# Kernel optimization log

Measured on AMD Instinct MI355X. Metric: run time of the kernel, lower is better.

The kernel has to match this reference:

```python
import jax, jax.numpy as jnp
import numpy as np

HEAD_SIZE = 64


def q_shift_multihead(x, ph, pw, head_dim=HEAD_SIZE, shift=1):
    # x: [B, T, C], T == ph*pw. Quarter-wise spatial shifts per head channel block.
    B, T, C = x.shape
    a = jnp.transpose(x, (0, 2, 1)).reshape(B, C // head_dim, head_dim, ph, pw)
    q = head_dim // 4
    out = jnp.zeros_like(a)
    out = out.at[:, :, 0:q, :, shift:].set(a[:, :, 0:q, :, :-shift])          # shift right in W
    out = out.at[:, :, q:2 * q, :, :-shift].set(a[:, :, q:2 * q, :, shift:])  # shift left in W
    out = out.at[:, :, 2 * q:3 * q, shift:, :].set(a[:, :, 2 * q:3 * q, :-shift, :])  # shift down in H
    out = out.at[:, :, 3 * q:, :-shift, :].set(a[:, :, 3 * q:, shift:, :])            # shift up in H
    return jnp.transpose(out.reshape(B, C, T), (0, 2, 1))


def wkv6(r, k, v, w, u):
    # RWKV-6 linear recurrence. r,k,v,w: [B,T,C]; u: [H, hs]. Decay applied as exp(-exp(w)).
    B, T, C = r.shape
    H, hs = C // HEAD_SIZE, HEAD_SIZE
    rh = jnp.transpose(r.reshape(B, T, H, hs), (1, 0, 2, 3))
    kh = jnp.transpose(k.reshape(B, T, H, hs), (1, 0, 2, 3))
    vh = jnp.transpose(v.reshape(B, T, H, hs), (1, 0, 2, 3))
    wh = jnp.exp(-jnp.exp(jnp.transpose(w.reshape(B, T, H, hs), (1, 0, 2, 3))))

    def step(S, inp):  # S: [B,H,hs(key j),hs(val i)]
        rt, kt, vt, wt = inp
        kv = kt[..., :, None] * vt[..., None, :]                # [B,H,hs,hs]
        y = jnp.einsum('bhj,bhji->bhi', rt, S + u[None, :, :, None] * kv)
        return wt[..., None] * S + kv, y

    S0 = jnp.zeros((B, H, hs, hs), r.dtype)
    _, ys = jax.lax.scan(step, S0, (rh, kh, vh, wh))
    return jnp.transpose(ys, (1, 0, 2, 3)).reshape(B, T, C)


def group_norm(x, weight, bias, n_groups, eps=1e-5):
    # x: [N, C]
    N, C = x.shape
    g = x.reshape(N, n_groups, C // n_groups)
    mu = g.mean(-1, keepdims=True)
    var = ((g - mu) ** 2).mean(-1, keepdims=True)
    g = (g - mu) / jnp.sqrt(var + eps)
    return g.reshape(N, C) * weight + bias


def setup_inputs() -> dict:
    key = jax.random.key(0)
    B, ph, pw, C = 8, 32, 32, 768
    T = ph * pw
    n_layer, layer_id = 12, 6
    H = C // HEAD_SIZE
    ks = jax.random.split(key, 10)
    x = jax.random.normal(ks[0], (B, T, C), jnp.float32)
    W_r = 0.02 * jax.random.normal(ks[1], (C, C), jnp.float32)
    W_k = 0.02 * jax.random.normal(ks[2], (C, C), jnp.float32)
    W_v = 0.02 * jax.random.normal(ks[3], (C, C), jnp.float32)
    W_g = 0.02 * jax.random.normal(ks[4], (C, C), jnp.float32)
    W_o = 0.02 * jax.random.normal(ks[5], (C, C), jnp.float32)
    r01 = layer_id / (n_layer - 1)
    r10 = 1.0 - layer_id / n_layer
    ddd = np.arange(C, dtype=np.float64) / C
    maa_x = jnp.asarray(1.0 - ddd ** r10, jnp.float32).reshape(1, 1, C)
    maa_w = maa_x
    maa_k = maa_x
    maa_v = jnp.asarray(1.0 - (ddd ** r10 + 0.3 * r01), jnp.float32).reshape(1, 1, C)
    maa_r = jnp.asarray(1.0 - ddd ** (0.5 * r10), jnp.float32).reshape(1, 1, C)
    maa_g = maa_r
    maa_w1 = jax.random.uniform(ks[6], (C, 32 * 5), jnp.float32, -1e-4, 1e-4)
    maa_w2 = jax.random.uniform(ks[7], (5, 32, C), jnp.float32, -1e-4, 1e-4)
    n = np.arange(C, dtype=np.float64)
    time_decay = jnp.asarray(-6 + 5 * (n / (C - 1)) ** (0.7 + 1.3 * r01), jnp.float32).reshape(1, 1, C)
    dec_w1 = jax.random.uniform(ks[8], (C, 64), jnp.float32, -1e-4, 1e-4)
    dec_w2 = jax.random.uniform(ks[9], (64, C), jnp.float32, -1e-4, 1e-4)
    zig = ((n + 1) % 3 - 1) * 0.1
    faaaa = jnp.asarray(r01 * (1 - n / (C - 1)) + zig, jnp.float32).reshape(H, HEAD_SIZE)
    ln_w = jnp.ones((C,), jnp.float32)
    ln_b = jnp.zeros((C,), jnp.float32)
    return dict(x=x, W_r=W_r, W_k=W_k, W_v=W_v, W_g=W_g, W_o=W_o,
                maa_x=maa_x, maa_w=maa_w, maa_k=maa_k, maa_v=maa_v, maa_r=maa_r, maa_g=maa_g,
                maa_w1=maa_w1, maa_w2=maa_w2, time_decay=time_decay,
                dec_w1=dec_w1, dec_w2=dec_w2, faaaa=faaaa, ln_w=ln_w, ln_b=ln_b,
                patch_h=ph, patch_w=pw)


def reference(x, W_r, W_k, W_v, W_g, W_o, maa_x, maa_w, maa_k, maa_v, maa_r, maa_g,
              maa_w1, maa_w2, time_decay, dec_w1, dec_w2, faaaa, ln_w, ln_b,
              patch_h, patch_w):
    B, T, C = x.shape
    xx = q_shift_multihead(x, patch_h, patch_w) - x
    xxx = x + xx * maa_x
    t = jnp.tanh(xxx @ maa_w1).reshape(B, T, 5, 32)
    m = jnp.einsum('btfr,frc->fbtc', t, maa_w2)  # [5,B,T,C]
    mw, mk, mv, mr, mg = m[0], m[1], m[2], m[3], m[4]
    xw = x + xx * (maa_w + mw)
    xk = x + xx * (maa_k + mk)
    xv = x + xx * (maa_v + mv)
    xr = x + xx * (maa_r + mr)
    xg = x + xx * (maa_g + mg)
    r = xr @ W_r.T
    k = xk @ W_k.T
    v = xv @ W_v.T
    g = jax.nn.relu(xg @ W_g.T)
    ww = jnp.tanh(xw @ dec_w1) @ dec_w2
    w = time_decay + ww
    y = wkv6(r, k, v, w, faaaa)
    y = group_norm(y.reshape(B * T, C), ln_w, ln_b, C // HEAD_SIZE).reshape(B, T, C)
    return (y * g) @ W_o.T
```

## Files before the change

kernel.cpp:

```cpp
#include <hip/hip_runtime.h>
#include <math.h>


#define EPI_NONE 0
#define EPI_TANH 1
#define EPI_RELU 2
#define EPI_BIAS 3

typedef float f32x4 __attribute__((ext_vector_type(4)));
typedef __bf16 bf16x8 __attribute__((ext_vector_type(8)));

__device__ __forceinline__ ushort f2bf(float x) {
  unsigned u = __float_as_uint(x);
  return (ushort)((u + 0x7fffu + ((u >> 16) & 1u)) >> 16);
}

#define GLDS16(gp, lp)                                                   \
  __builtin_amdgcn_global_load_lds(                                      \
      (const __attribute__((address_space(1))) void*)(gp),               \
      (__attribute__((address_space(3))) void*)(lp), 16, 0, 0)

__global__ __launch_bounds__(256) void k_qshift(
    const float* __restrict__ x, const float* __restrict__ maa_x,
    ushort* __restrict__ xxx_bf,
    int B, int T, int C, int ph, int pw) {
  long idx = (long)blockIdx.x * blockDim.x + threadIdx.x;
  long total = (long)B * T * C;
  if (idx >= total) return;
  int c = (int)(idx % C);
  long bt = idx / C;
  int t = (int)(bt % T);
  int quarter = (c & 63) >> 4;
  int hh = t / pw;
  int ww = t - hh * pw;
  long rowbase = (bt - t) * C;
  float sval = 0.f;
  int st = -1;
  if (quarter == 0)      { if (ww >= 1)      st = t - 1;  }
  else if (quarter == 1) { if (ww < pw - 1)  st = t + 1;  }
  else if (quarter == 2) { if (hh >= 1)      st = t - pw; }
  else                   { if (hh < ph - 1)  st = t + pw; }
  if (st >= 0) sval = x[rowbase + (long)st * C + c];
  float xval = x[idx];
  float d = sval - xval;
  xxx_bf[idx] = f2bf(xval + d * maa_x[c]);
}

__global__ __launch_bounds__(256) void k_wprep(
    const float* __restrict__ w1, const float* __restrict__ w2,
    const float* __restrict__ dw1, const float* __restrict__ dw2,
    ushort* __restrict__ maa1T, ushort* __restrict__ w2T,
    ushort* __restrict__ w1dT, ushort* __restrict__ w2dT) {
  int idx = blockIdx.x * 256 + threadIdx.x;
  if (idx < 196608) {
    int n = idx / 768, k = idx - n * 768;
    maa1T[idx] = f2bf(n < 160 ? w1[(size_t)k * 160 + n] : 0.f);
  } else if (idx < 196608 + 122880) {
    int j = idx - 196608;
    int c = j / 160, kk = j - c * 160;
    w2T[j] = f2bf(w2[(size_t)kk * 768 + c]);
  } else if (idx < 196608 + 122880 + 98304) {
    int j = idx - (196608 + 122880);
    int n = j / 768, k = j - n * 768;
    w1dT[j] = f2bf(n < 64 ? dw1[(size_t)k * 64 + n] : 0.f);
  } else {
    int j = idx - (196608 + 122880 + 98304);
    int n = j >> 6, k = j & 63;
    w2dT[j] = f2bf(dw2[(size_t)k * 768 + n]);
  }
}

__global__ __launch_bounds__(256) void k_mix5m(
    const ushort* __restrict__ t5b, const ushort* __restrict__ w2T,
    const float* __restrict__ x,
    const float* __restrict__ maa_w, const float* __restrict__ maa_k,
    const float* __restrict__ maa_v, const float* __restrict__ maa_r,
    const float* __restrict__ maa_g,
    ushort* __restrict__ xw, ushort* __restrict__ xk, ushort* __restrict__ xvb,
    ushort* __restrict__ xr, ushort* __restrict__ xg,
    int C, int T, int ph, int pw) {
  int tid = threadIdx.x;
  int lane = tid & 63, wid = tid >> 6;
  int m0 = blockIdx.y * 64, n0 = blockIdx.x * 128;
  int lm = lane & 15, lk = (lane >> 4) * 8;
  int rq = (lane >> 4) * 4;
  const ushort* ap = t5b + (size_t)(m0 + wid * 16 + lm) * 160 + lk;

  int stq[4][4];
#pragma unroll
  for (int q = 0; q < 4; q++) {
    int mr = m0 + wid * 16 + rq + q;
    int t = mr % T;
    int hh = t / pw, ww = t - hh * pw;
    stq[q][0] = (ww >= 1)      ? mr - 1  : -1;
    stq[q][1] = (ww < pw - 1)  ? mr + 1  : -1;
    stq[q][2] = (hh >= 1)      ? mr - pw : -1;
    stq[q][3] = (hh < ph - 1)  ? mr + pw : -1;
  }

  float xh[8][4], dh[8][4];
#pragma unroll
  for (int j = 0; j < 8; j++)
#pragma unroll
    for (int q = 0; q < 4; q++) {
      int mr = m0 + wid * 16 + rq + q;
      int col = n0 + j * 16 + lm;
      float xv = x[(size_t)mr * C + col];
      int sr = stq[q][j & 3];
      float sv = (sr >= 0) ? x[(size_t)sr * C + col] : 0.f;
      xh[j][q] = xv;
      dh[j][q] = sv - xv;
    }

#pragma unroll
  for (int f = 0; f < 5; f++) {
    bf16x8 af = *(const bf16x8*)(ap + f * 32);
    f32x4 acc[8];
#pragma unroll
    for (int j = 0; j < 8; j++) {
      bf16x8 bfj = *(const bf16x8*)(w2T +
          (size_t)(n0 + j * 16 + lm) * 160 + f * 32 + lk);
      acc[j] = __builtin_amdgcn_mfma_f32_16x16x32_bf16(
          af, bfj, (f32x4){0.f, 0.f, 0.f, 0.f}, 0, 0, 0);
    }
    const float* maa_f = (f == 0) ? maa_w : (f == 1) ? maa_k
                        : (f == 2) ? maa_v : (f == 3) ? maa_r : maa_g;
    ushort* dst = (f == 0) ? xw : (f == 1) ? xk
                 : (f == 2) ? xvb : (f == 3) ? xr : xg;
#pragma unroll
    for (int j = 0; j < 8; j++) {
      float mf = maa_f[n0 + j * 16 + lm];
#pragma unroll
      for (int q = 0; q < 4; q++) {
        size_t off = (size_t)(m0 + wid * 16 + rq + q) * C + (n0 + j * 16 + lm);
        dst[off] = f2bf(xh[j][q] + dh[j][q] * (mf + acc[j][q]));
      }
    }
  }
}

__global__ __launch_bounds__(256) void k_cvt5(
    const float* __restrict__ s0, const float* __restrict__ s1,
    const float* __restrict__ s2, const float* __restrict__ s3,
    const float* __restrict__ s4,
    ushort* __restrict__ d0, ushort* __restrict__ d1,
    ushort* __restrict__ d2, ushort* __restrict__ d3,
    ushort* __restrict__ d4, int n) {
  const float* s;
  ushort* d;
  switch (blockIdx.y) {
    case 0: s = s0; d = d0; break;
    case 1: s = s1; d = d1; break;
    case 2: s = s2; d = d2; break;
    case 3: s = s3; d = d3; break;
    default: s = s4; d = d4; break;
  }
  int i = (blockIdx.x * 256 + threadIdx.x) * 4;
  if (i >= n) return;
  float4 v = *(const float4*)(s + i);
  ushort4 o;
  o.x = f2bf(v.x); o.y = f2bf(v.y); o.z = f2bf(v.z); o.w = f2bf(v.w);
  *(ushort4*)(d + i) = o;
}

template <int EPI, bool NMASK, bool OBF16>
__global__ __launch_bounds__(256) void k_gemm_bf(
    const ushort* __restrict__ A, const ushort* __restrict__ W,
    const float* __restrict__ bias, void* __restrict__ Cm,
    int M, int N, int K) {
  __shared__ ushort Al[128 * 64];
  __shared__ ushort Bl[128 * 64];
  int nwg = gridDim.x * gridDim.y;
  int bid = blockIdx.y * gridDim.x + blockIdx.x;
  int swz = (nwg & 7) == 0 ? ((bid & 7) * (nwg >> 3) + (bid >> 3)) : bid;
  int bx = swz % gridDim.x, by = swz / gridDim.x;
  int m0 = by * 128, n0 = bx * 128;
  int tid = threadIdx.x;
  int lane = tid & 63, wave = tid >> 6;
  int wm = (wave >> 1) * 64, wn = (wave & 1) * 64;
  int lm = lane & 15, g = lane >> 4;
  f32x4 acc[4][4];
#pragma unroll
  for (int i = 0; i < 4; i++)
#pragma unroll
    for (int j = 0; j < 4; j++) acc[i][j] = (f32x4){0.f, 0.f, 0.f, 0.f};

  for (int k0 = 0; k0 < K; k0 += 64) {
#pragma unroll
    for (int i = 0; i < 4; i++) {
      int cid = tid + i * 256;
      int row = cid >> 3, p = cid & 7;
      int cq = p ^ (row & 7);
      GLDS16(A + (size_t)(m0 + row) * K + k0 + cq * 8, Al + cid * 8);
      GLDS16(W + (size_t)(n0 + row) * K + k0 + cq * 8, Bl + cid * 8);
    }
    __syncthreads();
#pragma unroll
    for (int s = 0; s < 2; s++) {
      bf16x8 af[4], bf[4];
#pragma unroll
      for (int i = 0; i < 4; i++) {
        int r = wm + i * 16 + lm;
        af[i] = *(const bf16x8*)&Al[r * 64 + (((s * 4 + g) ^ (r & 7)) * 8)];
        int rb = wn + i * 16 + lm;
        bf[i] = *(const bf16x8*)&Bl[rb * 64 + (((s * 4 + g) ^ (rb & 7)) * 8)];
      }
#pragma unroll
      for (int i = 0; i < 4; i++)
#pragma unroll
        for (int j = 0; j < 4; j++)
          acc[i][j] = __builtin_amdgcn_mfma_f32_16x16x32_bf16(
              af[i], bf[j], acc[i][j], 0, 0, 0);
    }
    __syncthreads();
  }
  int rq = (lane >> 4) * 4;
#pragma unroll
  for (int i = 0; i < 4; i++) {
#pragma unroll
    for (int j = 0; j < 4; j++) {
      int gn = n0 + wn + j * 16 + lm;
      if (NMASK && gn >= N) continue;
      float bv = (EPI == EPI_BIAS) ? bias[gn] : 0.f;
#pragma unroll
      for (int q = 0; q < 4; q++) {
        int gm = m0 + wm + i * 16 + rq + q;
        float val = acc[i][j][q];
        if (EPI == EPI_BIAS) val += bv;
        if (EPI == EPI_RELU) val = fmaxf(val, 0.f);
        if (EPI == EPI_TANH) val = tanhf(val);
        if (OBF16) ((ushort*)Cm)[(size_t)gm * N + gn] = f2bf(val);
        else       ((float*)Cm)[(size_t)gm * N + gn] = val;
      }
    }
  }
}

__global__ __launch_bounds__(256) void k_proj4(
    const ushort* __restrict__ A0, const ushort* __restrict__ A1,
    const ushort* __restrict__ A2, const ushort* __restrict__ A3,
    const ushort* __restrict__ W0, const ushort* __restrict__ W1,
    const ushort* __restrict__ W2, const ushort* __restrict__ W3,
    float* __restrict__ C0, float* __restrict__ C1,
    float* __restrict__ C2, float* __restrict__ C3,
    int M, int N, int K) {
  int nwg = gridDim.x;
  int bid = blockIdx.x;
  int swz = (bid & 7) * (nwg >> 3) + (bid >> 3);
  int nxt = N / 128;
  int per_z = (M / 128) * nxt;
  int z = swz / per_z;
  int rem = swz - z * per_z;
  int my = rem / nxt, nx = rem - my * nxt;
  const ushort* A = (z == 0) ? A0 : (z == 1) ? A1 : (z == 2) ? A2 : A3;
  const ushort* W = (z == 0) ? W0 : (z == 1) ? W1 : (z == 2) ? W2 : W3;
  float* Cm       = (z == 0) ? C0 : (z == 1) ? C1 : (z == 2) ? C2 : C3;
  __shared__ ushort Al[128 * 64];
  __shared__ ushort Bl[128 * 64];
  int tid = threadIdx.x;
  int m0 = my * 128, n0 = nx * 128;
  int lane = tid & 63, wave = tid >> 6;
  int wm = (wave >> 1) * 64, wn = (wave & 1) * 64;
  int lm = lane & 15, g = lane >> 4;
  f32x4 acc[4][4];
#pragma unroll
  for (int i = 0; i < 4; i++)
#pragma unroll
    for (int j = 0; j < 4; j++) acc[i][j] = (f32x4){0.f, 0.f, 0.f, 0.f};

  for (int k0 = 0; k0 < K; k0 += 64) {
#pragma unroll
    for (int i = 0; i < 4; i++) {
      int cid = tid + i * 256;
      int row = cid >> 3, p = cid & 7;
      int cq = p ^ (row & 7);
      GLDS16(A + (size_t)(m0 + row) * K + k0 + cq * 8, Al + cid * 8);
      GLDS16(W + (size_t)(n0 + row) * K + k0 + cq * 8, Bl + cid * 8);
    }
    __syncthreads();
#pragma unroll
    for (int s = 0; s < 2; s++) {
      bf16x8 af[4], bf[4];
#pragma unroll
      for (int i = 0; i < 4; i++) {
        int r = wm + i * 16 + lm;
        af[i] = *(const bf16x8*)&Al[r * 64 + (((s * 4 + g) ^ (r & 7)) * 8)];
        int rb = wn + i * 16 + lm;
        bf[i] = *(const bf16x8*)&Bl[rb * 64 + (((s * 4 + g) ^ (rb & 7)) * 8)];
      }
#pragma unroll
      for (int i = 0; i < 4; i++)
#pragma unroll
        for (int j = 0; j < 4; j++)
          acc[i][j] = __builtin_amdgcn_mfma_f32_16x16x32_bf16(
              af[i], bf[j], acc[i][j], 0, 0, 0);
    }
    __syncthreads();
  }
  bool relu = (z == 3);
  int rq = (lane >> 4) * 4;
#pragma unroll
  for (int i = 0; i < 4; i++) {
#pragma unroll
    for (int j = 0; j < 4; j++) {
      int gn = n0 + wn + j * 16 + lm;
#pragma unroll
      for (int q = 0; q < 4; q++) {
        int gm = m0 + wm + i * 16 + rq + q;
        float val = acc[i][j][q];
        if (relu) val = fmaxf(val, 0.f);
        Cm[(size_t)gm * N + gn] = val;
      }
    }
  }
}

__global__ __launch_bounds__(64) void k_wkv_pre(
    const float* __restrict__ r, const float* __restrict__ k,
    const float* __restrict__ w, const float* __restrict__ u,
    float* __restrict__ rt, float* __restrict__ kt,
    float* __restrict__ aL, float* __restrict__ pdiag,
    int B, int T, int C, int H, int L) {
  __shared__ float pls[64 * 65];
  int nch = T / L;
  int blk = blockIdx.x;
  int bh = blk / nch, c = blk - bh * nch;
  int b = bh / H, h = bh - b * H;
  int j = threadIdx.x;
  float uj = u[h * 64 + j];
  float cum = 0.f;
  long base = ((long)b * T + (long)c * L) * C + h * 64 + j;
  for (int tau = 0; tau < L; tau++) {
    long off = base + (long)tau * C;
    float wv = w[off];
    float rv = r[off];
    float kv = k[off];
    float e = expf(wv);
    rt[off] = rv * expf(-cum);
    cum += e;
    kt[off] = kv * expf(cum);
    pls[tau * 65 + j] = rv * uj * kv;
  }
  aL[((long)bh * nch + c) * 64 + j] = expf(-cum);
  __syncthreads();
  float s0 = 0.f, s1 = 0.f, s2 = 0.f, s3 = 0.f;
#pragma unroll
  for (int q = 0; q < 16; q++) {
    float4 p4 = *(const float4*)(pls + j * 65 + q * 4);
    s0 += p4.x; s1 += p4.y; s2 += p4.z; s3 += p4.w;
  }
  pdiag[(long)bh * T + c * L + j] = (s0 + s1) + (s2 + s3);
}

__global__ __launch_bounds__(256) void k_wkv_kv(
    const float* __restrict__ kt, const float* __restrict__ v,
    float* __restrict__ kvb, int B, int T, int C, int H, int L) {
  int nch = T / L;
  int blk = blockIdx.x;
  int bh = blk / nch, c = blk - bh * nch;
  int b = bh / H, h = bh - b * H;
  __shared__ float Ks[64 * 64];
  __shared__ float Vs[64 * 64];
  int tid = threadIdx.x;
  int lane = tid & 63, jg = tid >> 6;
  long cbase = ((long)b * T + (long)c * L) * C + h * 64;
#pragma unroll
  for (int i = 0; i < 4; i++) {
    int chunk = jg * 4 + i;
    int row = chunk * 4 + (lane >> 4);
    int cq = lane & 15;
    GLDS16(kt + cbase + (long)row * C + cq * 4, Ks + chunk * 256);
    GLDS16(v + cbase + (long)row * C + cq * 4, Vs + chunk * 256);
  }
  __syncthreads();
  float acc[16];
#pragma unroll
  for (int q = 0; q < 16; q++) acc[q] = 0.f;
  for (int s = 0; s < 64; s++) {
    float vi = Vs[s * 64 + lane];
#pragma unroll
    for (int q4 = 0; q4 < 4; q4++) {
      float4 kk = *(const float4*)(Ks + s * 64 + jg * 16 + q4 * 4);
      acc[q4 * 4 + 0] = fmaf(kk.x, vi, acc[q4 * 4 + 0]);
      acc[q4 * 4 + 1] = fmaf(kk.y, vi, acc[q4 * 4 + 1]);
      acc[q4 * 4 + 2] = fmaf(kk.z, vi, acc[q4 * 4 + 2]);
      acc[q4 * 4 + 3] = fmaf(kk.w, vi, acc[q4 * 4 + 3]);
    }
  }
  float* out = kvb + ((long)bh * nch + c) * 4096;
#pragma unroll
  for (int q = 0; q < 16; q++) out[(jg * 16 + q) * 64 + lane] = acc[q];
}

__global__ __launch_bounds__(256) void k_wkv_scan(
    const float* __restrict__ kvb, const float* __restrict__ aL,
    float* __restrict__ Scb, int nch) {
  int bh = blockIdx.x >> 4;
  int e = ((blockIdx.x & 15) << 8) + threadIdx.x;
  float S = 0.f;
  for (int c = 0; c < nch; c++) {
    long cb = ((long)bh * nch + c) * 4096 + e;
    Scb[cb] = S;
    S = aL[((long)bh * nch + c) * 64 + (e >> 6)] * (S + kvb[cb]);
  }
}

__global__ __launch_bounds__(256, 5) void k_wkv_intra(
    const float* __restrict__ rt, const float* __restrict__ kt,
    const float* __restrict__ v, const float* __restrict__ pdiag,
    const float* __restrict__ Scb, const float* __restrict__ g,
    const float* __restrict__ ln_w, const float* __restrict__ ln_b,
    ushort* __restrict__ z, int B, int T, int C, int H, int L) {
  int nch = T / L;
  int blk = blockIdx.x;
  int bh = blk / nch, c = blk - bh * nch;
  int b = bh / H, h = bh - b * H;
  __shared__ float TA[64 * 64];
  __shared__ float TB[64 * 64];
  int tid = threadIdx.x;
  int lane = tid & 63, wid = tid >> 6;
  int tau = lane;
  long cbase = ((long)b * T + (long)c * L) * C + h * 64;
  const float* scp = Scb + ((long)bh * nch + c) * 4096;

#pragma unroll
  for (int i = 0; i < 4; i++) {
    int chunk = wid * 4 + i;
    int row = chunk * 4 + (lane >> 4);
    int cq = lane & 15;
    GLDS16(rt + cbase + (long)row * C + ((cq ^ (row & 15)) * 4),
           TA + chunk * 256);
    GLDS16(kt + cbase + (long)row * C + cq * 4, TB + chunk * 256);
  }
  __syncthreads();

  float4 rreg[16];
#pragma unroll
  for (int q = 0; q < 16; q++)
    rreg[q] = *(const float4*)(TA + tau * 64 + ((q ^ (tau & 15)) * 4));
  float pd = pdiag[(long)bh * T + c * L + tau];
  __syncthreads();

#pragma unroll
  for (int i = 0; i < 4; i++) {
    int chunk = wid * 4 + i;
    int row = chunk * 4 + (lane >> 4);
    GLDS16(v + cbase + (long)row * C + (lane & 15) * 4, TA + chunk * 256);
  }

  __builtin_amdgcn_s_setprio(1);
#pragma unroll 2
  for (int ss = 0; ss < 16; ss++) {
    int s = wid * 16 + ss;
    float a0 = 0.f, a1 = 0.f, a2 = 0.f, a3 = 0.f;
#pragma unroll
    for (int q = 0; q < 16; q++) {
      float4 kk = *(const float4*)(TB + s * 64 + q * 4);
      a0 = fmaf(rreg[q].x, kk.x, a0);
      a1 = fmaf(rreg[q].y, kk.y, a1);
      a2 = fmaf(rreg[q].z, kk.z, a2);
      a3 = fmaf(rreg[q].w, kk.w, a3);
    }
    float a = (a0 + a1) + (a2 + a3);
    float val = (s < tau) ? a : (s == tau ? pd : 0.f);
    TB[s * 64 + tau] = val;
  }
  __builtin_amdgcn_s_setprio(0);
  __syncthreads();

  int row0 = wid * 16 + ((lane >> 4) << 2);
  int c0 = (lane & 15) * 4;
  float4 acc0 = {0.f, 0.f, 0.f, 0.f};
  float4 acc1 = {0.f, 0.f, 0.f, 0.f};
  float4 acc2 = {0.f, 0.f, 0.f, 0.f};
  float4 acc3 = {0.f, 0.f, 0.f, 0.f};
#define FMA1(A, P, V4)                 \
  A.x = fmaf(P, V4.x, A.x);            \
  A.y = fmaf(P, V4.y, A.y);            \
  A.z = fmaf(P, V4.z, A.z);            \
  A.w = fmaf(P, V4.w, A.w);
  __builtin_amdgcn_s_setprio(1);
#pragma unroll 4
  for (int j = 0; j < 64; j++) {
    float4 pp = *(const float4*)(TB + j * 64 + row0);
    float4 vv = *(const float4*)(TA + j * 64 + c0);
    FMA1(acc0, pp.x, vv);
    FMA1(acc1, pp.y, vv);
    FMA1(acc2, pp.z, vv);
    FMA1(acc3, pp.w, vv);
  }
  __builtin_amdgcn_s_setprio(0);
  __syncthreads();

#define WRQ(SG)                                                          \
  {                                                                      \
    _Pragma("unroll") for (int qq = 0; qq < 16; qq++) {                  \
      const float* rp = (const float*)&rreg[(SG) * 4 + (qq >> 2)];       \
      TA[((SG) * 16 + qq) * 64 + tau] = rp[qq & 3];                      \
    }                                                                    \
  }
  if (wid == 0)      WRQ(0)
  else if (wid == 1) WRQ(1)
  else if (wid == 2) WRQ(2)
  else               WRQ(3)
#undef WRQ
  __syncthreads();

  __builtin_amdgcn_s_setprio(1);
#pragma unroll 4
  for (int j = 0; j < 64; j++) {
    float4 rr = *(const float4*)(TA + j * 64 + row0);
    float4 ssv = *(const float4*)(scp + j * 64 + c0);
    FMA1(acc0, rr.x, ssv);
    FMA1(acc1, rr.y, ssv);
    FMA1(acc2, rr.z, ssv);
    FMA1(acc3, rr.w, ssv);
  }
  __builtin_amdgcn_s_setprio(0);
#undef FMA1

  float4 lw4 = *(const float4*)(ln_w + h * 64 + c0);
  float4 lb4 = *(const float4*)(ln_b + h * 64 + c0);
#define GNROW(A, m)                                                        \
  {                                                                        \
    float s1 = (A.x + A.y) + (A.z + A.w);                                  \
    s1 += __shfl_xor(s1, 1, 64);                                           \
    s1 += __shfl_xor(s1, 2, 64);                                           \
    s1 += __shfl_xor(s1, 4, 64);                                           \
    s1 += __shfl_xor(s1, 8, 64);                                           \
    float mu = s1 * (1.f / 64.f);                                          \
    float4 dd;                                                             \
    dd.x = A.x - mu; dd.y = A.y - mu; dd.z = A.z - mu; dd.w = A.w - mu;    \
    float s2 = (dd.x * dd.x + dd.y * dd.y) + (dd.z * dd.z + dd.w * dd.w);  \
    s2 += __shfl_xor(s2, 1, 64);                                           \
    s2 += __shfl_xor(s2, 2, 64);                                           \
    s2 += __shfl_xor(s2, 4, 64);                                           \
    s2 += __shfl_xor(s2, 8, 64);                                           \
    float rstd = rsqrtf(s2 * (1.f / 64.f) + 1e-5f);                        \
    long off = cbase + (long)(row0 + m) * C + c0;                          \
    float4 g4 = *(const float4*)(g + off);                                 \
    ushort4 ob;                                                            \
    ob.x = f2bf((dd.x * rstd * lw4.x + lb4.x) * g4.x);                     \
    ob.y = f2bf((dd.y * rstd * lw4.y + lb4.y) * g4.y);                     \
    ob.z = f2bf((dd.z * rstd * lw4.z + lb4.z) * g4.z);                     \
    ob.w = f2bf((dd.w * rstd * lw4.w + lb4.w) * g4.w);                     \
    *(ushort4*)(z + off) = ob;                                             \
  }
  GNROW(acc0, 0)
  GNROW(acc1, 1)
  GNROW(acc2, 2)
  GNROW(acc3, 3)
#undef GNROW
}

extern "C" void kernel_launch(void* const* d_in, const int* in_sizes, int n_in,
                              void* d_out, int out_size, void* d_ws, size_t ws_size,
                              hipStream_t stream) {
  const int B = 8, T = 1024, C = 768, H = 12, ph = 32, pw = 32;
  const int M = B * T;
  const int L = 64, NCH = T / L;

  const float* x        = (const float*)d_in[0];
  const float* W_r      = (const float*)d_in[1];
  const float* W_k      = (const float*)d_in[2];
  const float* W_v      = (const float*)d_in[3];
  const float* W_g      = (const float*)d_in[4];
  const float* W_o      = (const float*)d_in[5];
  const float* maa_x    = (const float*)d_in[6];
  const float* maa_w    = (const float*)d_in[7];
  const float* maa_k    = (const float*)d_in[8];
  const float* maa_v    = (const float*)d_in[9];
  const float* maa_r    = (const float*)d_in[10];
  const float* maa_g    = (const float*)d_in[11];
  const float* maa_w1   = (const float*)d_in[12];
  const float* maa_w2   = (const float*)d_in[13];
  const float* time_dec = (const float*)d_in[14];
  const float* dec_w1   = (const float*)d_in[15];
  const float* dec_w2   = (const float*)d_in[16];
  const float* faaaa    = (const float*)d_in[17];
  const float* ln_w     = (const float*)d_in[18];
  const float* ln_b     = (const float*)d_in[19];

  float* ws = (float*)d_ws;
  const size_t S = (size_t)M * C;
  float* F0 = ws + 0 * S;
  float* F1 = ws + 1 * S;
  float* F2 = ws + 2 * S;
  float* F3 = ws + 3 * S;
  float* F4 = ws + 4 * S;
  float* F5 = ws + 5 * S;
  float* F6 = ws + 6 * S;
  float* t5    = ws + 7 * S;
  float* t6    = t5 + (size_t)M * 160;
  float* aLb   = t6 + (size_t)M * 64;
  float* pdiag = aLb + (size_t)B * H * NCH * 64;
  float* dec_t = pdiag + (size_t)B * H * T;

  ushort* xxx_bf = (ushort*)F1;
  ushort* xw_bf = (ushort*)F2;
  ushort* xr_bf = (ushort*)F5;
  ushort* xk_bf = xr_bf + S;
  ushort* xv_bf = (ushort*)F6;
  ushort* xg_bf = xv_bf + S;
  ushort* z_bf  = (ushort*)F6;
  ushort* t5b   = (ushort*)t5;
  ushort* t_bf  = (ushort*)dec_t;
  ushort* w2T   = t_bf + (size_t)M * 64;
  float* kvb = F0;
  float* Scb = F1;
  const int WSZ = C * C;
  ushort* wr_bf = (ushort*)t5;
  ushort* wk_bf = wr_bf + WSZ;
  ushort* wv_bf = wk_bf + WSZ;
  ushort* wg_bf = wv_bf + WSZ;
  ushort* wo_bf = (ushort*)t6;
  ushort* maa1T = wo_bf + WSZ;
  ushort* w1dT  = maa1T + 256 * 768;
  ushort* w2dT  = w1dT + 128 * 768;

  {
    long total = (long)M * C;
    k_qshift<<<(int)((total + 255) / 256), 256, 0, stream>>>(
        x, maa_x, xxx_bf, B, T, C, ph, pw);
  }
  {
    k_wprep<<<1824, 256, 0, stream>>>(maa_w1, maa_w2, dec_w1, dec_w2,
                                      maa1T, w2T, w1dT, w2dT);
    dim3 grid(2, M / 128);
    k_gemm_bf<EPI_TANH, true, true><<<grid, 256, 0, stream>>>(
        xxx_bf, maa1T, nullptr, t5b, M, 160, C);
  }
  {
    dim3 grid(C / 128, M / 64);
    k_mix5m<<<grid, 256, 0, stream>>>(t5b, w2T, x, maa_w, maa_k, maa_v,
                                      maa_r, maa_g, xw_bf, xk_bf, xv_bf, xr_bf,
                                      xg_bf, C, T, ph, pw);
  }
  {
    dim3 grid((WSZ / 4 + 255) / 256, 5);
    k_cvt5<<<grid, 256, 0, stream>>>(W_r, W_k, W_v, W_g, W_o,
                                     wr_bf, wk_bf, wv_bf, wg_bf, wo_bf, WSZ);
  }
  {
    k_proj4<<<(C / 128) * (M / 128) * 4, 256, 0, stream>>>(
        xr_bf, xk_bf, xv_bf, xg_bf, wr_bf, wk_bf, wv_bf, wg_bf,
        F0, F1, F3, F4, M, C, C);
  }
  {
    dim3 g1(1, M / 128);
    k_gemm_bf<EPI_TANH, true, true><<<g1, 256, 0, stream>>>(
        xw_bf, w1dT, nullptr, t_bf, M, 64, C);
    dim3 g2(C / 128, M / 128);
    k_gemm_bf<EPI_BIAS, false, false><<<g2, 256, 0, stream>>>(
        t_bf, w2dT, time_dec, F2, M, C, 64);
  }
  k_wkv_pre<<<B * H * NCH, 64, 0, stream>>>(F0, F1, F2, faaaa, F5, F2,
                                            aLb, pdiag, B, T, C, H, L);
  k_wkv_kv<<<B * H * NCH, 256, 0, stream>>>(F2, F3, kvb, B, T, C, H, L);
  k_wkv_scan<<<B * H * 16, 256, 0, stream>>>(kvb, aLb, Scb, NCH);
  k_wkv_intra<<<B * H * NCH, 256, 0, stream>>>(F5, F2, F3, pdiag, Scb, F4,
                                               ln_w, ln_b, z_bf, B, T, C, H, L);
  {
    dim3 grid(C / 128, M / 128);
    k_gemm_bf<EPI_NONE, false, false><<<grid, 256, 0, stream>>>(
        z_bf, wo_bf, nullptr, (float*)d_out, M, C, C);
  }
}
```

Before: 417.1 us.

## Process two chunks per WKV intra block with prefetch of next chunk's r/k

Each k_wkv_intra block now handles two consecutive chunks, using a third shared-memory tile to prefetch the second chunk's r and k while the first chunk is computed. This halves the grid and is meant to overlap global loads with compute within a block. In exchange, LDS use rises to 48KB per block and the occupancy hint drops from 5 to 3 blocks per CU, which reduces latency hiding across blocks and leaves fewer blocks in the grid (768).

```diff
diff --git a/kernel.cpp b/kernel.cpp
--- a/kernel.cpp
+++ b/kernel.cpp
@@ -405,123 +405,123 @@
   }
 }
 
-__global__ __launch_bounds__(256, 5) void k_wkv_intra(
+__global__ __launch_bounds__(256, 3) void k_wkv_intra(
     const float* __restrict__ rt, const float* __restrict__ kt,
     const float* __restrict__ v, const float* __restrict__ pdiag,
     const float* __restrict__ Scb, const float* __restrict__ g,
     const float* __restrict__ ln_w, const float* __restrict__ ln_b,
     ushort* __restrict__ z, int B, int T, int C, int H, int L) {
   int nch = T / L;
+  int npair = nch >> 1;
   int blk = blockIdx.x;
-  int bh = blk / nch, c = blk - bh * nch;
+  int bh = blk / npair, cp = blk - bh * npair;
+  int c0 = cp * 2;
   int b = bh / H, h = bh - b * H;
   __shared__ float TA[64 * 64];
   __shared__ float TB[64 * 64];
+  __shared__ float TC[64 * 64];
   int tid = threadIdx.x;
   int lane = tid & 63, wid = tid >> 6;
   int tau = lane;
-  long cbase = ((long)b * T + (long)c * L) * C + h * 64;
-  const float* scp = Scb + ((long)bh * nch + c) * 4096;
+  long cbase0 = ((long)b * T + (long)c0 * L) * C + h * 64;
+  long cbase1 = cbase0 + (long)L * C;
+  const float* scp0 = Scb + ((long)bh * nch + c0) * 4096;
+  const float* scp1 = scp0 + 4096;
+  int row0 = wid * 16 + ((lane >> 4) << 2);
+  int c0v = (lane & 15) * 4;
+  float4 lw4 = *(const float4*)(ln_w + h * 64 + c0v);
+  float4 lb4 = *(const float4*)(ln_b + h * 64 + c0v);
 
 #pragma unroll
   for (int i = 0; i < 4; i++) {
     int chunk = wid * 4 + i;
     int row = chunk * 4 + (lane >> 4);
     int cq = lane & 15;
-    GLDS16(rt + cbase + (long)row * C + ((cq ^ (row & 15)) * 4),
-           TA + chunk * 256);
-    GLDS16(kt + cbase + (long)row * C + cq * 4, TB + chunk * 256);
+    GLDS16(rt + cbase0 + (long)row * C + ((cq ^ (row & 15)) * 4),
+           TC + chunk * 256);
+    GLDS16(kt + cbase0 + (long)row * C + cq * 4, TB + chunk * 256);
   }
   __syncthreads();
 
   float4 rreg[16];
 #pragma unroll
   for (int q = 0; q < 16; q++)
-    rreg[q] = *(const float4*)(TA + tau * 64 + ((q ^ (tau & 15)) * 4));
-  float pd = pdiag[(long)bh * T + c * L + tau];
+    rreg[q] = *(const float4*)(TC + tau * 64 + ((q ^ (tau & 15)) * 4));
+  float pd0 = pdiag[(long)bh * T + c0 * L + tau];
+  float pd1 = pdiag[(long)bh * T + (c0 + 1) * L + tau];
   __syncthreads();
 
 #pragma unroll
   for (int i = 0; i < 4; i++) {
     int chunk = wid * 4 + i;
     int row = chunk * 4 + (lane >> 4);
-    GLDS16(v + cbase + (long)row * C + (lane & 15) * 4, TA + chunk * 256);
-  }
-
-  __builtin_amdgcn_s_setprio(1);
-#pragma unroll 2
-  for (int ss = 0; ss < 16; ss++) {
-    int s = wid * 16 + ss;
-    float a0 = 0.f, a1 = 0.f, a2 = 0.f, a3 = 0.f;
-#pragma unroll
-    for (int q = 0; q < 16; q++) {
-      float4 kk = *(const float4*)(TB + s * 64 + q * 4);
-      a0 = fmaf(rreg[q].x, kk.x, a0);
-      a1 = fmaf(rreg[q].y, kk.y, a1);
-      a2 = fmaf(rreg[q].z, kk.z, a2);
-      a3 = fmaf(rreg[q].w, kk.w, a3);
-    }
-    float a = (a0 + a1) + (a2 + a3);
-    float val = (s < tau) ? a : (s == tau ? pd : 0.f);
-    TB[s * 64 + tau] = val;
-  }
+    int cq = lane & 15;
+    GLDS16(v + cbase0 + (long)row * C + cq * 4, TA + chunk * 256);
+    GLDS16(rt + cbase1 + (long)row * C + ((cq ^ (row & 15)) * 4),
+           TC + chunk * 256);
+  }
+
+#define PHASE1(PD)                                                       \
+  __builtin_amdgcn_s_setprio(1);                                         \
+  _Pragma("unroll 2") for (int ss = 0; ss < 16; ss++) {                  \
+    int s = wid * 16 + ss;                                               \
+    float a0 = 0.f, a1 = 0.f, a2 = 0.f, a3 = 0.f;                        \
+    _Pragma("unroll") for (int q = 0; q < 16; q++) {                     \
+      float4 kk = *(const float4*)(TB + s * 64 + q * 4);                 \
+      a0 = fmaf(rreg[q].x, kk.x, a0);                                    \
+      a1 = fmaf(rreg[q].y, kk.y, a1);                                    \
+      a2 = fmaf(rreg[q].z, kk.z, a2);                                    \
+      a3 = fmaf(rreg[q].w, kk.w, a3);                                    \
+    }                                                                    \
+    float a = (a0 + a1) + (a2 + a3);                                     \
+    TB[s * 64 + tau] = (s < tau) ? a : (s == tau ? (PD) : 0.f);          \
+  }                                                                      \
   __builtin_amdgcn_s_setprio(0);
-  __syncthreads();
-
-  int row0 = wid * 16 + ((lane >> 4) << 2);
-  int c0 = (lane & 15) * 4;
-  float4 acc0 = {0.f, 0.f, 0.f, 0.f};
-  float4 acc1 = {0.f, 0.f, 0.f, 0.f};
-  float4 acc2 = {0.f, 0.f, 0.f, 0.f};
-  float4 acc3 = {0.f, 0.f, 0.f, 0.f};
+
 #define FMA1(A, P, V4)                 \
   A.x = fmaf(P, V4.x, A.x);            \
   A.y = fmaf(P, V4.y, A.y);            \
   A.z = fmaf(P, V4.z, A.z);            \
   A.w = fmaf(P, V4.w, A.w);
-  __builtin_amdgcn_s_setprio(1);
-#pragma unroll 4
-  for (int j = 0; j < 64; j++) {
-    float4 pp = *(const float4*)(TB + j * 64 + row0);
-    float4 vv = *(const float4*)(TA + j * 64 + c0);
-    FMA1(acc0, pp.x, vv);
-    FMA1(acc1, pp.y, vv);
-    FMA1(acc2, pp.z, vv);
-    FMA1(acc3, pp.w, vv);
-  }
+
+#define PASSA                                                            \
+  __builtin_amdgcn_s_setprio(1);                                         \
+  _Pragma("unroll 4") for (int j = 0; j < 64; j++) {                     \
+    float4 pp = *(const float4*)(TB + j * 64 + row0);                    \
+    float4 vv = *(const float4*)(TA + j * 64 + c0v);                     \
+    FMA1(acc0, pp.x, vv);                                                \
+    FMA1(acc1, pp.y, vv);                                                \
+    FMA1(acc2, pp.z, vv);                                                \
+    FMA1(acc3, pp.w, vv);                                                \
+  }                                                                      \
   __builtin_amdgcn_s_setprio(0);
-  __syncthreads();
-
+
+#define PASSB(SCP)                                                       \
+  __builtin_amdgcn_s_setprio(1);                                         \
+  _Pragma("unroll 4") for (int j = 0; j < 64; j++) {                     \
+    float4 rr = *(const float4*)(TA + j * 64 + row0);                    \
+    float4 ssv = *(const float4*)((SCP) + j * 64 + c0v);                 \
+    FMA1(acc0, rr.x, ssv);                                               \
+    FMA1(acc1, rr.y, ssv);                                               \
+    FMA1(acc2, rr.z, ssv);                                               \
+    FMA1(acc3, rr.w, ssv);                                               \
+  }                                                                      \
+  __builtin_amdgcn_s_setprio(0);
+
+#define WRQ_ALL                                                          \
+  {                                                                      \
+    if (wid == 0) { WRQ(0) }                                             \
+    else if (wid == 1) { WRQ(1) }                                        \
+    else if (wid == 2) { WRQ(2) }                                        \
+    else { WRQ(3) }                                                      \
+  }
 #define WRQ(SG)                                                          \
-  {                                                                      \
-    _Pragma("unroll") for (int qq = 0; qq < 16; qq++) {                  \
-      const float* rp = (const float*)&rreg[(SG) * 4 + (qq >> 2)];       \
-      TA[((SG) * 16 + qq) * 64 + tau] = rp[qq & 3];                      \
-    }                                                                    \
-  }
-  if (wid == 0)      WRQ(0)
-  else if (wid == 1) WRQ(1)
-  else if (wid == 2) WRQ(2)
-  else               WRQ(3)
-#undef WRQ
-  __syncthreads();
-
-  __builtin_amdgcn_s_setprio(1);
-#pragma unroll 4
-  for (int j = 0; j < 64; j++) {
-    float4 rr = *(const float4*)(TA + j * 64 + row0);
-    float4 ssv = *(const float4*)(scp + j * 64 + c0);
-    FMA1(acc0, rr.x, ssv);
-    FMA1(acc1, rr.y, ssv);
-    FMA1(acc2, rr.z, ssv);
-    FMA1(acc3, rr.w, ssv);
-  }
-  __builtin_amdgcn_s_setprio(0);
-#undef FMA1
-
-  float4 lw4 = *(const float4*)(ln_w + h * 64 + c0);
-  float4 lb4 = *(const float4*)(ln_b + h * 64 + c0);
-#define GNROW(A, m)                                                        \
+  _Pragma("unroll") for (int qq = 0; qq < 16; qq++) {                    \
+    const float* rp = (const float*)&rreg[(SG) * 4 + (qq >> 2)];         \
+    TA[((SG) * 16 + qq) * 64 + tau] = rp[qq & 3];                        \
+  }
+
+#define GNROW(A, m, CBASE)                                                 \
   {                                                                        \
     float s1 = (A.x + A.y) + (A.z + A.w);                                  \
     s1 += __shfl_xor(s1, 1, 64);                                           \
@@ -537,7 +537,7 @@
     s2 += __shfl_xor(s2, 4, 64);                                           \
     s2 += __shfl_xor(s2, 8, 64);                                           \
     float rstd = rsqrtf(s2 * (1.f / 64.f) + 1e-5f);                        \
-    long off = cbase + (long)(row0 + m) * C + c0;                          \
+    long off = (CBASE) + (long)(row0 + m) * C + c0v;                       \
     float4 g4 = *(const float4*)(g + off);                                 \
     ushort4 ob;                                                            \
     ob.x = f2bf((dd.x * rstd * lw4.x + lb4.x) * g4.x);                     \
@@ -546,10 +546,65 @@
     ob.w = f2bf((dd.w * rstd * lw4.w + lb4.w) * g4.w);                     \
     *(ushort4*)(z + off) = ob;                                             \
   }
-  GNROW(acc0, 0)
-  GNROW(acc1, 1)
-  GNROW(acc2, 2)
-  GNROW(acc3, 3)
+
+  PHASE1(pd0)
+  __syncthreads();
+  {
+    float4 acc0 = {0.f, 0.f, 0.f, 0.f};
+    float4 acc1 = {0.f, 0.f, 0.f, 0.f};
+    float4 acc2 = {0.f, 0.f, 0.f, 0.f};
+    float4 acc3 = {0.f, 0.f, 0.f, 0.f};
+    PASSA
+    __syncthreads();
+#pragma unroll
+    for (int i = 0; i < 4; i++) {
+      int chunk = wid * 4 + i;
+      int row = chunk * 4 + (lane >> 4);
+      int cq = lane & 15;
+      GLDS16(kt + cbase1 + (long)row * C + cq * 4, TB + chunk * 256);
+    }
+    WRQ_ALL
+    __syncthreads();
+    PASSB(scp0)
+    GNROW(acc0, 0, cbase0)
+    GNROW(acc1, 1, cbase0)
+    GNROW(acc2, 2, cbase0)
+    GNROW(acc3, 3, cbase0)
+  }
+#pragma unroll
+  for (int q = 0; q < 16; q++)
+    rreg[q] = *(const float4*)(TC + tau * 64 + ((q ^ (tau & 15)) * 4));
+  __syncthreads();
+
+#pragma unroll
+  for (int i = 0; i < 4; i++) {
+    int chunk = wid * 4 + i;
+    int row = chunk * 4 + (lane >> 4);
+    GLDS16(v + cbase1 + (long)row * C + (lane & 15) * 4, TA + chunk * 256);
+  }
+  PHASE1(pd1)
+  __syncthreads();
+  {
+    float4 acc0 = {0.f, 0.f, 0.f, 0.f};
+    float4 acc1 = {0.f, 0.f, 0.f, 0.f};
+    float4 acc2 = {0.f, 0.f, 0.f, 0.f};
+    float4 acc3 = {0.f, 0.f, 0.f, 0.f};
+    PASSA
+    __syncthreads();
+    WRQ_ALL
+    __syncthreads();
+    PASSB(scp1)
+    GNROW(acc0, 0, cbase1)
+    GNROW(acc1, 1, cbase1)
+    GNROW(acc2, 2, cbase1)
+    GNROW(acc3, 3, cbase1)
+  }
+#undef PHASE1
+#undef FMA1
+#undef PASSA
+#undef PASSB
+#undef WRQ
+#undef WRQ_ALL
 #undef GNROW
 }
 
@@ -658,8 +713,8 @@
                                             aLb, pdiag, B, T, C, H, L);
   k_wkv_kv<<<B * H * NCH, 256, 0, stream>>>(F2, F3, kvb, B, T, C, H, L);
   k_wkv_scan<<<B * H * 16, 256, 0, stream>>>(kvb, aLb, Scb, NCH);
-  k_wkv_intra<<<B * H * NCH, 256, 0, stream>>>(F5, F2, F3, pdiag, Scb, F4,
-                                               ln_w, ln_b, z_bf, B, T, C, H, L);
+  k_wkv_intra<<<B * H * (NCH / 2), 256, 0, stream>>>(
+      F5, F2, F3, pdiag, Scb, F4, ln_w, ln_b, z_bf, B, T, C, H, L);
   {
     dim3 grid(C / 128, M / 128);
     k_gemm_bf<EPI_NONE, false, false><<<grid, 256, 0, stream>>>(
```

New measurement: 421.7 us. Within noise of the previous version (+1.1%).

## Restructure wkv intra-chunk kernel with transposed LDS tiles and fused P·V + R·S loop

Applied to the files above, without the earlier changes.

Rewrites the intra-chunk WKV kernel. K and R are staged transposed into padded LDS tiles, and the masked attention matrix is computed with a 4x4 register-blocked outer product instead of per-lane dot products. The P·V and R·S accumulations are merged into one loop that reads V and S directly from global memory, which removes two syncs and the LDS rewrite of R. This uses more LDS, with three padded tiles instead of two, and lowers the occupancy hint from 5 to 3. It also drops the async global-to-LDS loads and the priority hints.

```diff
diff --git a/kernel.cpp b/kernel.cpp
--- a/kernel.cpp
+++ b/kernel.cpp
@@ -405,7 +405,7 @@
   }
 }
 
-__global__ __launch_bounds__(256, 5) void k_wkv_intra(
+__global__ __launch_bounds__(256, 3) void k_wkv_intra(
     const float* __restrict__ rt, const float* __restrict__ kt,
     const float* __restrict__ v, const float* __restrict__ pdiag,
     const float* __restrict__ Scb, const float* __restrict__ g,
@@ -415,112 +415,100 @@
   int blk = blockIdx.x;
   int bh = blk / nch, c = blk - bh * nch;
   int b = bh / H, h = bh - b * H;
-  __shared__ float TA[64 * 64];
-  __shared__ float TB[64 * 64];
+  __shared__ float KtT[64 * 68];
+  __shared__ float RtT[64 * 68];
+  __shared__ float Pt[64 * 68];
   int tid = threadIdx.x;
   int lane = tid & 63, wid = tid >> 6;
-  int tau = lane;
   long cbase = ((long)b * T + (long)c * L) * C + h * 64;
   const float* scp = Scb + ((long)bh * nch + c) * 4096;
 
-#pragma unroll
-  for (int i = 0; i < 4; i++) {
-    int chunk = wid * 4 + i;
-    int row = chunk * 4 + (lane >> 4);
-    int cq = lane & 15;
-    GLDS16(rt + cbase + (long)row * C + ((cq ^ (row & 15)) * 4),
-           TA + chunk * 256);
-    GLDS16(kt + cbase + (long)row * C + cq * 4, TB + chunk * 256);
+  {
+    int t0 = (tid >> 4) * 4;
+    int c0s = (tid & 15) * 4;
+    float4 ka[4], ra[4];
+#pragma unroll
+    for (int i = 0; i < 4; i++) {
+      ka[i] = *(const float4*)(kt + cbase + (long)(t0 + i) * C + c0s);
+      ra[i] = *(const float4*)(rt + cbase + (long)(t0 + i) * C + c0s);
+    }
+#pragma unroll
+    for (int j = 0; j < 4; j++) {
+      float4 ko, ro;
+      ko.x = ka[0][j]; ko.y = ka[1][j]; ko.z = ka[2][j]; ko.w = ka[3][j];
+      ro.x = ra[0][j]; ro.y = ra[1][j]; ro.z = ra[2][j]; ro.w = ra[3][j];
+      *(float4*)(KtT + (c0s + j) * 68 + t0) = ko;
+      *(float4*)(RtT + (c0s + j) * 68 + t0) = ro;
+    }
   }
   __syncthreads();
 
-  float4 rreg[16];
-#pragma unroll
-  for (int q = 0; q < 16; q++)
-    rreg[q] = *(const float4*)(TA + tau * 64 + ((q ^ (tau & 15)) * 4));
-  float pd = pdiag[(long)bh * T + c * L + tau];
+  {
+    int s0 = (tid >> 4) * 4;
+    int tau0 = (tid & 15) * 4;
+    float4 pd4 = *(const float4*)(pdiag + (long)bh * T + c * L + tau0);
+    float p00 = 0.f, p01 = 0.f, p02 = 0.f, p03 = 0.f;
+    float p10 = 0.f, p11 = 0.f, p12 = 0.f, p13 = 0.f;
+    float p20 = 0.f, p21 = 0.f, p22 = 0.f, p23 = 0.f;
+    float p30 = 0.f, p31 = 0.f, p32 = 0.f, p33 = 0.f;
+#pragma unroll 4
+    for (int cc = 0; cc < 64; cc++) {
+      float4 kq = *(const float4*)(KtT + cc * 68 + s0);
+      float4 rq = *(const float4*)(RtT + cc * 68 + tau0);
+      p00 = fmaf(kq.x, rq.x, p00); p01 = fmaf(kq.x, rq.y, p01);
+      p02 = fmaf(kq.x, rq.z, p02); p03 = fmaf(kq.x, rq.w, p03);
+      p10 = fmaf(kq.y, rq.x, p10); p11 = fmaf(kq.y, rq.y, p11);
+      p12 = fmaf(kq.y, rq.z, p12); p13 = fmaf(kq.y, rq.w, p13);
+      p20 = fmaf(kq.z, rq.x, p20); p21 = fmaf(kq.z, rq.y, p21);
+      p22 = fmaf(kq.z, rq.z, p22); p23 = fmaf(kq.z, rq.w, p23);
+      p30 = fmaf(kq.w, rq.x, p30); p31 = fmaf(kq.w, rq.y, p31);
+      p32 = fmaf(kq.w, rq.z, p32); p33 = fmaf(kq.w, rq.w, p33);
+    }
+#define PMASK(PI0, PI1, PI2, PI3, I)                                       \
+    {                                                                      \
+      int s = s0 + (I);                                                    \
+      float4 o;                                                            \
+      o.x = (s < tau0 + 0) ? PI0 : (s == tau0 + 0 ? pd4.x : 0.f);          \
+      o.y = (s < tau0 + 1) ? PI1 : (s == tau0 + 1 ? pd4.y : 0.f);          \
+      o.z = (s < tau0 + 2) ? PI2 : (s == tau0 + 2 ? pd4.z : 0.f);          \
+      o.w = (s < tau0 + 3) ? PI3 : (s == tau0 + 3 ? pd4.w : 0.f);          \
+      *(float4*)(Pt + s * 68 + tau0) = o;                                  \
+    }
+    PMASK(p00, p01, p02, p03, 0)
+    PMASK(p10, p11, p12, p13, 1)
+    PMASK(p20, p21, p22, p23, 2)
+    PMASK(p30, p31, p32, p33, 3)
+#undef PMASK
+  }
   __syncthreads();
 
-#pragma unroll
-  for (int i = 0; i < 4; i++) {
-    int chunk = wid * 4 + i;
-    int row = chunk * 4 + (lane >> 4);
-    GLDS16(v + cbase + (long)row * C + (lane & 15) * 4, TA + chunk * 256);
-  }
-
-  __builtin_amdgcn_s_setprio(1);
-#pragma unroll 2
-  for (int ss = 0; ss < 16; ss++) {
-    int s = wid * 16 + ss;
-    float a0 = 0.f, a1 = 0.f, a2 = 0.f, a3 = 0.f;
-#pragma unroll
-    for (int q = 0; q < 16; q++) {
-      float4 kk = *(const float4*)(TB + s * 64 + q * 4);
-      a0 = fmaf(rreg[q].x, kk.x, a0);
-      a1 = fmaf(rreg[q].y, kk.y, a1);
-      a2 = fmaf(rreg[q].z, kk.z, a2);
-      a3 = fmaf(rreg[q].w, kk.w, a3);
-    }
-    float a = (a0 + a1) + (a2 + a3);
-    float val = (s < tau) ? a : (s == tau ? pd : 0.f);
-    TB[s * 64 + tau] = val;
-  }
-  __builtin_amdgcn_s_setprio(0);
-  __syncthreads();
-
   int row0 = wid * 16 + ((lane >> 4) << 2);
-  int c0 = (lane & 15) * 4;
+  int c0v = (lane & 15) * 4;
   float4 acc0 = {0.f, 0.f, 0.f, 0.f};
   float4 acc1 = {0.f, 0.f, 0.f, 0.f};
   float4 acc2 = {0.f, 0.f, 0.f, 0.f};
   float4 acc3 = {0.f, 0.f, 0.f, 0.f};
-#define FMA1(A, P, V4)                 \
-  A.x = fmaf(P, V4.x, A.x);            \
-  A.y = fmaf(P, V4.y, A.y);            \
-  A.z = fmaf(P, V4.z, A.z);            \
-  A.w = fmaf(P, V4.w, A.w);
-  __builtin_amdgcn_s_setprio(1);
+  const float* vp = v + cbase + c0v;
+#define FMA2(A, P, V4, R, S4)                          \
+  A.x = fmaf(P, V4.x, fmaf(R, S4.x, A.x));             \
+  A.y = fmaf(P, V4.y, fmaf(R, S4.y, A.y));             \
+  A.z = fmaf(P, V4.z, fmaf(R, S4.z, A.z));             \
+  A.w = fmaf(P, V4.w, fmaf(R, S4.w, A.w));
 #pragma unroll 4
   for (int j = 0; j < 64; j++) {
-    float4 pp = *(const float4*)(TB + j * 64 + row0);
-    float4 vv = *(const float4*)(TA + j * 64 + c0);
-    FMA1(acc0, pp.x, vv);
-    FMA1(acc1, pp.y, vv);
-    FMA1(acc2, pp.z, vv);
-    FMA1(acc3, pp.w, vv);
-  }
-  __builtin_amdgcn_s_setprio(0);
-  __syncthreads();
-
-#define WRQ(SG)                                                          \
-  {                                                                      \
-    _Pragma("unroll") for (int qq = 0; qq < 16; qq++) {                  \
-      const float* rp = (const float*)&rreg[(SG) * 4 + (qq >> 2)];       \
-      TA[((SG) * 16 + qq) * 64 + tau] = rp[qq & 3];                      \
-    }                                                                    \
-  }
-  if (wid == 0)      WRQ(0)
-  else if (wid == 1) WRQ(1)
-  else if (wid == 2) WRQ(2)
-  else               WRQ(3)
-#undef WRQ
-  __syncthreads();
-
-  __builtin_amdgcn_s_setprio(1);
-#pragma unroll 4
-  for (int j = 0; j < 64; j++) {
-    float4 rr = *(const float4*)(TA + j * 64 + row0);
-    float4 ssv = *(const float4*)(scp + j * 64 + c0);
-    FMA1(acc0, rr.x, ssv);
-    FMA1(acc1, rr.y, ssv);
-    FMA1(acc2, rr.z, ssv);
-    FMA1(acc3, rr.w, ssv);
-  }
-  __builtin_amdgcn_s_setprio(0);
-#undef FMA1
-
-  float4 lw4 = *(const float4*)(ln_w + h * 64 + c0);
-  float4 lb4 = *(const float4*)(ln_b + h * 64 + c0);
+    float4 pp = *(const float4*)(Pt + j * 68 + row0);
+    float4 rr = *(const float4*)(RtT + j * 68 + row0);
+    float4 vv = *(const float4*)(vp + (long)j * C);
+    float4 ssv = *(const float4*)(scp + j * 64 + c0v);
+    FMA2(acc0, pp.x, vv, rr.x, ssv);
+    FMA2(acc1, pp.y, vv, rr.y, ssv);
+    FMA2(acc2, pp.z, vv, rr.z, ssv);
+    FMA2(acc3, pp.w, vv, rr.w, ssv);
+  }
+#undef FMA2
+
+  float4 lw4 = *(const float4*)(ln_w + h * 64 + c0v);
+  float4 lb4 = *(const float4*)(ln_b + h * 64 + c0v);
 #define GNROW(A, m)                                                        \
   {                                                                        \
     float s1 = (A.x + A.y) + (A.z + A.w);                                  \
@@ -537,7 +525,7 @@
     s2 += __shfl_xor(s2, 4, 64);                                           \
     s2 += __shfl_xor(s2, 8, 64);                                           \
     float rstd = rsqrtf(s2 * (1.f / 64.f) + 1e-5f);                        \
-    long off = cbase + (long)(row0 + m) * C + c0;                          \
+    long off = cbase + (long)(row0 + m) * C + c0v;                         \
     float4 g4 = *(const float4*)(g + off);                                 \
     ushort4 ob;                                                            \
     ob.x = f2bf((dd.x * rstd * lw4.x + lb4.x) * g4.x);                     \
@@ -658,8 +646,8 @@
                                             aLb, pdiag, B, T, C, H, L);
   k_wkv_kv<<<B * H * NCH, 256, 0, stream>>>(F2, F3, kvb, B, T, C, H, L);
   k_wkv_scan<<<B * H * 16, 256, 0, stream>>>(kvb, aLb, Scb, NCH);
-  k_wkv_intra<<<B * H * NCH, 256, 0, stream>>>(F5, F2, F3, pdiag, Scb, F4,
-                                               ln_w, ln_b, z_bf, B, T, C, H, L);
+  k_wkv_intra<<<B * H * NCH, 256, 0, stream>>>(
+      F5, F2, F3, pdiag, Scb, F4, ln_w, ln_b, z_bf, B, T, C, H, L);
   {
     dim3 grid(C / 128, M / 128);
     k_gemm_bf<EPI_NONE, false, false><<<grid, 256, 0, stream>>>(
```

Result: faster. 385.8 us (-7.5%).
